# Kernel optimization log

Hardware: AMD Instinct MI355X
Metric: run time of the kernel (lower is better)

The kernel has to match this reference:

```python
import jax, jax.numpy as jnp
import numpy as np

B, S, H = 2, 1024, 4544
NH, HD = 71, 64          # 71 query heads, head_dim 64, 1 shared kv head (multi-query)
THETA = 10000.0
NEG_INF = -1e9


def setup_inputs() -> dict:
    key = jax.random.key(0)
    k1, k2, k3 = jax.random.split(key, 3)
    hidden_states = jax.random.normal(k1, (B, S, H), dtype=jnp.float32)
    W_qkv = jax.random.normal(k2, (H, H + 2 * HD), dtype=jnp.float32) * 0.02
    W_dense = jax.random.normal(k3, (H, H), dtype=jnp.float32) * 0.02
    causal = jnp.tril(jnp.ones((S, S), dtype=bool))
    attention_mask = jnp.where(causal, 0.0, NEG_INF).astype(jnp.float32)[None, None]  # [1,1,S,S]
    position_ids = jnp.arange(S, dtype=jnp.int32)[None]  # [1,S]
    return {"hidden_states": hidden_states, "W_qkv": W_qkv, "W_dense": W_dense,
            "attention_mask": attention_mask, "position_ids": position_ids}


def _rope_cos_sin(position_ids):
    # HF FalconRotaryEmbedding: inv_freq over even dims, emb = cat(freqs, freqs)
    inv_freq = 1.0 / (THETA ** (jnp.arange(0, HD, 2, dtype=jnp.float32) / HD))
    freqs = position_ids.astype(jnp.float32)[..., None] * inv_freq  # [1,S,HD/2]
    emb = jnp.concatenate([freqs, freqs], axis=-1)                  # [1,S,HD]
    return jnp.cos(emb)[:, None], jnp.sin(emb)[:, None]             # [1,1,S,HD]


def _rotate_half(x):
    return jnp.concatenate([-x[..., HD // 2:], x[..., :HD // 2]], axis=-1)


def reference(hidden_states, W_qkv, W_dense, attention_mask, position_ids):
    # fused QKV projection (bias=False for Falcon-7B)
    fused = hidden_states @ W_qkv                       # [B,S,(NH+2)*HD]
    fused = fused.reshape(B, S, NH + 2, HD)
    q = jnp.transpose(fused[:, :, :NH], (0, 2, 1, 3))          # [B,NH,S,HD]
    k = jnp.transpose(fused[:, :, NH:NH + 1], (0, 2, 1, 3))    # [B,1,S,HD]
    v = jnp.transpose(fused[:, :, NH + 1:], (0, 2, 1, 3))      # [B,1,S,HD]

    cos, sin = _rope_cos_sin(position_ids)
    q = q * cos + _rotate_half(q) * sin
    k = k * cos + _rotate_half(k) * sin

    # scores: shared kv head broadcasts across the 71 query heads
    scores = jnp.matmul(q, jnp.swapaxes(k, -1, -2)) * (1.0 / np.sqrt(HD))  # [B,NH,S,S]
    probs = jax.nn.softmax(scores + attention_mask, axis=-1)
    attn = jnp.matmul(probs, v)                                            # [B,NH,S,HD]

    attn = jnp.transpose(attn, (0, 2, 1, 3)).reshape(B, S, NH * HD)
    return attn @ W_dense
```

## Files before the change

### kernel.cpp

```cpp
#include <hip/hip_runtime.h>

typedef unsigned short u16;
using f32x4  = __attribute__((ext_vector_type(4))) float;
using f32x16 = __attribute__((ext_vector_type(16))) float;
using s16x8  = __attribute__((ext_vector_type(8))) short;

static __device__ __forceinline__ u16 f2b(float f) {
  unsigned int u = __builtin_bit_cast(unsigned int, f);
  u = (u + 0x7fffu + ((u >> 16) & 1u)) >> 16;
  return (u16)u;
}
static __device__ __forceinline__ float b2f(u16 h) {
  unsigned int u = ((unsigned int)h) << 16;
  return __builtin_bit_cast(float, u);
}
static __device__ __forceinline__ unsigned int cvtpk(float lo, float hi) {
  unsigned int r;
  asm("v_cvt_pk_bf16_f32 %0, %1, %2" : "=v"(r) : "v"(lo), "v"(hi));
  return r;
}
static __device__ __forceinline__ void gload16(const void* g, void* l) {
  __builtin_amdgcn_global_load_lds(
      (const __attribute__((address_space(1))) void*)g,
      (__attribute__((address_space(3))) void*)l, 16, 0, 0);
}

__global__ __launch_bounds__(256) void conv_bf16(
    const float* __restrict__ in, u16* __restrict__ out, int n8)
{
  int i = blockIdx.x * 256 + threadIdx.x;
  if (i >= n8) return;
  float4 a = *(const float4*)(in + (size_t)i * 8);
  float4 b = *(const float4*)(in + (size_t)i * 8 + 4);
  __align__(16) u16 tmp[8] = {f2b(a.x), f2b(a.y), f2b(a.z), f2b(a.w),
                              f2b(b.x), f2b(b.y), f2b(b.z), f2b(b.w)};
  *(uint4*)(out + (size_t)i * 8) = *(const uint4*)tmp;
}

__global__ __launch_bounds__(256) void transpose_conv(
    const float* __restrict__ W, u16* __restrict__ Wt, int K, int N)
{
  __shared__ u16 tile[64][72];
  const int t = threadIdx.x;
  const int n0 = blockIdx.x * 64, k0 = blockIdx.y * 64;
  #pragma unroll
  for (int i = 0; i < 4; ++i) {
    int idx = i * 256 + t;
    int r = idx >> 4;
    int c = (idx & 15) << 2;
    float4 v = make_float4(0.f, 0.f, 0.f, 0.f);
    if (n0 + c < N) v = *(const float4*)(W + (size_t)(k0 + r) * N + n0 + c);
    tile[r][c + 0] = f2b(v.x);
    tile[r][c + 1] = f2b(v.y);
    tile[r][c + 2] = f2b(v.z);
    tile[r][c + 3] = f2b(v.w);
  }
  __syncthreads();
  #pragma unroll
  for (int i = 0; i < 2; ++i) {
    int idx = i * 256 + t;
    int rn = idx >> 3;
    int c8 = (idx & 7) << 3;
    __align__(16) u16 tmp[8];
    #pragma unroll
    for (int j = 0; j < 8; ++j) tmp[j] = tile[c8 + j][rn];
    *(uint4*)(Wt + (size_t)(n0 + rn) * K + k0 + c8) = *(const uint4*)tmp;
  }
}

template<int MODE>
__global__ __launch_bounds__(256) void gemm_bt(
    const u16* __restrict__ A, const u16* __restrict__ B,
    float* __restrict__ Cptr,
    u16* __restrict__ qo, u16* __restrict__ ko, u16* __restrict__ vo,
    const int* __restrict__ pos,
    int M, int N, int K, int NBX)
{
  __shared__ __align__(16) u16 aLds[2][128 * 64];
  __shared__ __align__(16) u16 bLds[2][128 * 64];

  const int t = threadIdx.x, lane = t & 63, w = t >> 6;
  const int lr = lane & 15, lg = lane >> 4;
  const int wr = w >> 1, wc = w & 1;

  const int bid = blockIdx.x;
  const int qq  = gridDim.x >> 3;
  const int swz = (bid & 7) * qq + (bid >> 3);
  const int m0 = (swz / NBX) * 128, n0 = (swz % NBX) * 128;

  const int srow = lane >> 3;
  const int ssw  = ((lane & 7) ^ srow) << 3;

  f32x4 acc[4][4] = {};
  const int nk = K >> 6;

#define STAGE(buf, tt) do {                                                   \
    size_t kq_ = (size_t)(tt) << 6;                                           \
    _Pragma("unroll")                                                         \
    for (int u_ = 0; u_ < 4; ++u_) {                                          \
      int row_ = u_ * 32 + w * 8 + srow;                                      \
      gload16(A + (size_t)(m0 + row_) * K + kq_ + ssw,                        \
              (char*)&aLds[buf][0] + u_ * 4096 + w * 1024);                   \
      gload16(B + (size_t)(n0 + row_) * K + kq_ + ssw,                        \
              (char*)&bLds[buf][0] + u_ * 4096 + w * 1024);                   \
    }                                                                         \
  } while (0)

  STAGE(0, 0);
  for (int kt = 0; kt < nk; ++kt) {
    const int cur = kt & 1;
    if (kt + 1 < nk) {
      STAGE(cur ^ 1, kt + 1);
      asm volatile("s_waitcnt vmcnt(8)" ::: "memory");
    } else {
      asm volatile("s_waitcnt vmcnt(0)" ::: "memory");
    }
    __builtin_amdgcn_s_barrier();
    __builtin_amdgcn_sched_barrier(0);
    const char* ab = (const char*)&aLds[cur][0];
    const char* bb = (const char*)&bLds[cur][0];
    s16x8 af[4], bf[4];
    #pragma unroll
    for (int kk = 0; kk < 2; ++kk) {
      const int csw = ((kk << 6) | (lg << 4)) ^ ((lr & 7) << 4);
      #pragma unroll
      for (int m = 0; m < 4; ++m)
        af[m] = *(const s16x8*)(ab + (wr * 64 + m * 16 + lr) * 128 + csw);
      #pragma unroll
      for (int n = 0; n < 4; ++n)
        bf[n] = *(const s16x8*)(bb + (wc * 64 + n * 16 + lr) * 128 + csw);
      #pragma unroll
      for (int m = 0; m < 4; ++m)
        #pragma unroll
        for (int n = 0; n < 4; ++n)
          acc[m][n] = __builtin_amdgcn_mfma_f32_16x16x32_bf16(af[m], bf[n], acc[m][n], 0, 0, 0);
    }
    __builtin_amdgcn_s_barrier();
  }
#undef STAGE

  if constexpr (MODE == 0) {
    #pragma unroll
    for (int m = 0; m < 4; ++m) {
      int row = m0 + wr * 64 + m * 16 + lg * 4;
      #pragma unroll
      for (int n = 0; n < 4; ++n) {
        int col = n0 + wc * 64 + n * 16 + lr;
        if (col < N) {
          #pragma unroll
          for (int r = 0; r < 4; ++r)
            Cptr[(size_t)(row + r) * N + col] = acc[m][n][r];
        }
      }
    }
  } else {
    const int h = (n0 + wc * 64) >> 6;
    if (h > 72) return;
    const float inv0 = exp2f(-0.41524101186092029f * (float)lr);
    const float inv1 = exp2f(-0.41524101186092029f * (float)(16 + lr));
    #pragma unroll
    for (int m = 0; m < 4; ++m) {
      #pragma unroll
      for (int r = 0; r < 4; ++r) {
        int row = m0 + wr * 64 + m * 16 + lg * 4 + r;
        int b = row >> 10, s = row & 1023;
        if (h == 72) {
          #pragma unroll
          for (int n = 0; n < 4; ++n) {
            int d = n * 16 + lr;
            vo[((size_t)b * 64 + d) * 1024 + s] = f2b(acc[m][n][r]);
          }
        } else {
          float p = (float)pos[s];
          float sn0, cs0, sn1, cs1;
          __sincosf(p * inv0, &sn0, &cs0);
          __sincosf(p * inv1, &sn1, &cs1);
          #pragma unroll
          for (int n = 0; n < 4; ++n) {
            float cs  = (n & 1) ? cs1 : cs0;
            float sn  = (n & 1) ? sn1 : sn0;
            float sgn = (n < 2) ? -1.f : 1.f;
            float val = acc[m][n][r] * cs + sgn * acc[m][n ^ 2][r] * sn;
            int d = n * 16 + lr;
            if (h < 71)
              qo[((size_t)(b * 71 + h) * 1024 + s) * 64 + d] = f2b(val);
            else
              ko[((size_t)b * 1024 + s) * 64 + d] = f2b(val);
          }
        }
      }
    }
  }
}

__global__ __launch_bounds__(128) void attn_kernel(
    const u16* __restrict__ q, const u16* __restrict__ kx,
    const u16* __restrict__ vT, u16* __restrict__ attnO)
{
  const int t = threadIdx.x, lane = t & 63, w = t >> 6;
  const int lq  = lane & 31;
  const int hi  = lane >> 5;
  const int hi4 = hi << 2;
  const int pair = blockIdx.x, h = blockIdx.y, b = blockIdx.z;
  const int qt = w ? (31 - pair) : pair;
  const int q0 = qt * 32;

  const u16* qbase = q + ((size_t)(b * 71 + h) * 1024 + q0 + lq) * 64 + hi * 8;
  s16x8 qf[4];
  #pragma unroll
  for (int kt = 0; kt < 4; ++kt) qf[kt] = *(const s16x8*)(qbase + kt * 16);

  f32x16 o0 = {}, o1 = {};
  float m = -1e30f, l = 0.f;

  const u16* kbase  = kx + ((size_t)b * 1024 + lq) * 64 + hi * 8;
  const u16* vbase0 = vT + ((size_t)b * 64 + lq) * 1024 + hi * 8;
  const u16* vbase1 = vbase0 + 32 * 1024;

  for (int it = 0; it <= qt; ++it) {
    const int kv0 = it * 32;
    s16x8 kf[4];
    #pragma unroll
    for (int kt = 0; kt < 4; ++kt)
      kf[kt] = *(const s16x8*)(kbase + (size_t)kv0 * 64 + kt * 16);
    s16x8 v00 = *(const s16x8*)(vbase0 + kv0);
    s16x8 v01 = *(const s16x8*)(vbase0 + kv0 + 16);
    s16x8 v10 = *(const s16x8*)(vbase1 + kv0);
    s16x8 v11 = *(const s16x8*)(vbase1 + kv0 + 16);

    f32x16 sa = {}, sb = {};
    sa = __builtin_amdgcn_mfma_f32_32x32x16_bf16(kf[0], qf[0], sa, 0, 0, 0);
    sb = __builtin_amdgcn_mfma_f32_32x32x16_bf16(kf[1], qf[1], sb, 0, 0, 0);
    sa = __builtin_amdgcn_mfma_f32_32x32x16_bf16(kf[2], qf[2], sa, 0, 0, 0);
    sb = __builtin_amdgcn_mfma_f32_32x32x16_bf16(kf[3], qf[3], sb, 0, 0, 0);

    float s[16];
    float pmax = -1e30f;
    if (it == qt) {
      #pragma unroll
      for (int r = 0; r < 16; ++r) {
        int R = (r & 3) + ((r >> 2) << 3) + hi4;
        s[r] = (R > lq) ? -1e30f : (sa[r] + sb[r]) * 0.125f;
        pmax = fmaxf(pmax, s[r]);
      }
    } else {
      #pragma unroll
      for (int r = 0; r < 16; ++r) {
        s[r] = (sa[r] + sb[r]) * 0.125f;
        pmax = fmaxf(pmax, s[r]);
      }
    }
    pmax = fmaxf(pmax, __shfl_xor(pmax, 32));

    if (!__all(pmax <= m + 8.f)) {
      float mn = fmaxf(m, pmax);
      float corr = __expf(m - mn);
      m = mn;
      l *= corr;
      #pragma unroll
      for (int r = 0; r < 16; ++r) {
        float c2 = __shfl(corr, (r & 3) + ((r >> 2) << 3) + hi4);
        o0[r] *= c2; o1[r] *= c2;
      }
    }

    float p[16], sum = 0.f;
    #pragma unroll
    for (int r = 0; r < 16; ++r) { p[r] = __expf(s[r] - m); sum += p[r]; }
    sum += __shfl_xor(sum, 32);
    l += sum;

    unsigned int a0 = cvtpk(p[0], p[1]),   a1 = cvtpk(p[2], p[3]);
    unsigned int b0 = cvtpk(p[4], p[5]),   b1 = cvtpk(p[6], p[7]);
    asm("v_permlane32_swap_b32 %0, %1" : "+v"(a0), "+v"(b0));
    asm("v_permlane32_swap_b32 %0, %1" : "+v"(a1), "+v"(b1));
    unsigned int c0 = cvtpk(p[8], p[9]),   c1 = cvtpk(p[10], p[11]);
    unsigned int d0 = cvtpk(p[12], p[13]), d1 = cvtpk(p[14], p[15]);
    asm("v_permlane32_swap_b32 %0, %1" : "+v"(c0), "+v"(d0));
    asm("v_permlane32_swap_b32 %0, %1" : "+v"(c1), "+v"(d1));
    union { unsigned int wd[4]; s16x8 v; } palo, pahi;
    palo.wd[0] = a0; palo.wd[1] = a1; palo.wd[2] = b0; palo.wd[3] = b1;
    pahi.wd[0] = c0; pahi.wd[1] = c1; pahi.wd[2] = d0; pahi.wd[3] = d1;

    o0 = __builtin_amdgcn_mfma_f32_32x32x16_bf16(palo.v, v00, o0, 0, 0, 0);
    o0 = __builtin_amdgcn_mfma_f32_32x32x16_bf16(pahi.v, v01, o0, 0, 0, 0);
    o1 = __builtin_amdgcn_mfma_f32_32x32x16_bf16(palo.v, v10, o1, 0, 0, 0);
    o1 = __builtin_amdgcn_mfma_f32_32x32x16_bf16(pahi.v, v11, o1, 0, 0, 0);
  }

  float linv = 1.f / l;
  #pragma unroll
  for (int r = 0; r < 16; ++r) {
    int R = (r & 3) + ((r >> 2) << 3) + hi4;
    float c2 = __shfl(linv, R);
    size_t base = ((size_t)(b * 1024 + q0 + R) * 71 + h) * 64;
    attnO[base + lq]      = f2b(o0[r] * c2);
    attnO[base + 32 + lq] = f2b(o1[r] * c2);
  }
}

extern "C" void kernel_launch(void* const* d_in, const int* in_sizes, int n_in,
                              void* d_out, int out_size, void* d_ws, size_t ws_size,
                              hipStream_t stream) {
  const float* hidden = (const float*)d_in[0];
  const float* Wqkv   = (const float*)d_in[1];
  const float* Wdense = (const float*)d_in[2];
  const int*   pos    = (const int*)d_in[4];
  float* out = (float*)d_out;

  char* wsp = (char*)d_ws;
  u16* Wt    = (u16*)(wsp);
  u16* A1    = (u16*)(wsp + 43040768);
  u16* qws   = (u16*)(wsp + 43040768 + 18612224);
  u16* kws   = (u16*)(wsp + 43040768 + 18612224 + 18612224);
  u16* vws   = (u16*)(wsp + 43040768 + 18612224 + 18612224 + 262144);
  u16* attnw = A1;

  conv_bf16<<<4544, 256, 0, stream>>>(hidden, A1, 2048 * 4544 / 8);
  transpose_conv<<<dim3(74, 71), 256, 0, stream>>>(Wqkv, Wt, 4544, 4672);
  gemm_bt<2><<<592, 256, 0, stream>>>(A1, Wt, nullptr, qws, kws, vws, pos,
                                      2048, 4672, 4544, 37);
  transpose_conv<<<dim3(72, 71), 256, 0, stream>>>(Wdense, Wt, 4544, 4544);
  attn_kernel<<<dim3(16, 71, 2), 128, 0, stream>>>(qws, kws, vws, attnw);
  gemm_bt<0><<<576, 256, 0, stream>>>(attnw, Wt, out, nullptr, nullptr, nullptr,
                                      nullptr, 2048, 4544, 4544, 36);
}
```

Measured before the change: 451.7 us.

## Switch GEMM to triple-buffered LDS pipeline with BK=32 tiles

The GEMM main loop moves from a double-buffered BK=64 pipeline to a triple-buffered BK=32 pipeline, prefetching two stages ahead to hide global-load latency. It also drops the XOR swizzle on the LDS layout, storing rows as plain 64-byte lines. This halves the work per barrier and doubles the number of loop iterations and barriers. Removing the swizzle may introduce LDS bank conflicts on the fragment reads.

```diff
diff --git a/kernel.cpp b/kernel.cpp
--- a/kernel.cpp
+++ b/kernel.cpp
@@ -76,8 +76,8 @@
     const int* __restrict__ pos,
     int M, int N, int K, int NBX)
 {
-  __shared__ __align__(16) u16 aLds[2][128 * 64];
-  __shared__ __align__(16) u16 bLds[2][128 * 64];
+  __shared__ __align__(16) u16 aLds[3][128 * 32];
+  __shared__ __align__(16) u16 bLds[3][128 * 32];
 
   const int t = threadIdx.x, lane = t & 63, w = t >> 6;
   const int lr = lane & 15, lg = lane >> 4;
@@ -88,54 +88,56 @@
   const int swz = (bid & 7) * qq + (bid >> 3);
   const int m0 = (swz / NBX) * 128, n0 = (swz % NBX) * 128;
 
-  const int srow = lane >> 3;
-  const int ssw  = ((lane & 7) ^ srow) << 3;
+  const int srow = lane >> 2;
+  const int skc  = (lane & 3) << 3;
 
   f32x4 acc[4][4] = {};
-  const int nk = K >> 6;
+  const int nk = K >> 5;
 
 #define STAGE(buf, tt) do {                                                   \
-    size_t kq_ = (size_t)(tt) << 6;                                           \
+    size_t kq_ = (size_t)(tt) << 5;                                           \
     _Pragma("unroll")                                                         \
-    for (int u_ = 0; u_ < 4; ++u_) {                                          \
-      int row_ = u_ * 32 + w * 8 + srow;                                      \
-      gload16(A + (size_t)(m0 + row_) * K + kq_ + ssw,                        \
-              (char*)&aLds[buf][0] + u_ * 4096 + w * 1024);                   \
-      gload16(B + (size_t)(n0 + row_) * K + kq_ + ssw,                        \
-              (char*)&bLds[buf][0] + u_ * 4096 + w * 1024);                   \
+    for (int i_ = 0; i_ < 2; ++i_) {                                          \
+      int row_ = i_ * 64 + w * 16 + srow;                                     \
+      gload16(A + (size_t)(m0 + row_) * K + kq_ + skc,                        \
+              (char*)&aLds[buf][0] + i_ * 4096 + w * 1024);                   \
+      gload16(B + (size_t)(n0 + row_) * K + kq_ + skc,                        \
+              (char*)&bLds[buf][0] + i_ * 4096 + w * 1024);                   \
     }                                                                         \
   } while (0)
 
   STAGE(0, 0);
+  if (nk > 1) STAGE(1, 1);
+
+  int cur = 0;
   for (int kt = 0; kt < nk; ++kt) {
-    const int cur = kt & 1;
-    if (kt + 1 < nk) {
-      STAGE(cur ^ 1, kt + 1);
+    const int nx2 = cur >= 1 ? cur - 1 : cur + 2;
+    if (kt + 2 < nk) {
+      STAGE(nx2, kt + 2);
       asm volatile("s_waitcnt vmcnt(8)" ::: "memory");
+    } else if (kt + 1 < nk) {
+      asm volatile("s_waitcnt vmcnt(4)" ::: "memory");
     } else {
       asm volatile("s_waitcnt vmcnt(0)" ::: "memory");
     }
     __builtin_amdgcn_s_barrier();
     __builtin_amdgcn_sched_barrier(0);
-    const char* ab = (const char*)&aLds[cur][0];
-    const char* bb = (const char*)&bLds[cur][0];
+    const u16* ab = &aLds[cur][0];
+    const u16* bb = &bLds[cur][0];
     s16x8 af[4], bf[4];
     #pragma unroll
-    for (int kk = 0; kk < 2; ++kk) {
-      const int csw = ((kk << 6) | (lg << 4)) ^ ((lr & 7) << 4);
-      #pragma unroll
-      for (int m = 0; m < 4; ++m)
-        af[m] = *(const s16x8*)(ab + (wr * 64 + m * 16 + lr) * 128 + csw);
+    for (int m = 0; m < 4; ++m)
+      af[m] = *(const s16x8*)(ab + (wr * 64 + m * 16 + lr) * 32 + lg * 8);
+    #pragma unroll
+    for (int n = 0; n < 4; ++n)
+      bf[n] = *(const s16x8*)(bb + (wc * 64 + n * 16 + lr) * 32 + lg * 8);
+    #pragma unroll
+    for (int m = 0; m < 4; ++m)
       #pragma unroll
       for (int n = 0; n < 4; ++n)
-        bf[n] = *(const s16x8*)(bb + (wc * 64 + n * 16 + lr) * 128 + csw);
-      #pragma unroll
-      for (int m = 0; m < 4; ++m)
-        #pragma unroll
-        for (int n = 0; n < 4; ++n)
-          acc[m][n] = __builtin_amdgcn_mfma_f32_16x16x32_bf16(af[m], bf[n], acc[m][n], 0, 0, 0);
-    }
+        acc[m][n] = __builtin_amdgcn_mfma_f32_16x16x32_bf16(af[m], bf[n], acc[m][n], 0, 0, 0);
     __builtin_amdgcn_s_barrier();
+    cur = cur < 2 ? cur + 1 : 0;
   }
 #undef STAGE
 
```

Result: faster. 387.2 us (-14.3%).
